# Optimization experiments

Measured on AMD Instinct MI355X. Metric: run time of the kernel, lower is better.

## Reference

```python
import jax, jax.numpy as jnp
import numpy as np

NEG_BIG = -9e15  # matches torch -9000000000000000.0

def setup_inputs() -> dict:
    key = jax.random.key(0)
    k1, k2, k3, k4 = jax.random.split(key, 4)
    B, N, F_IN, F_OUT = 8, 2048, 128, 64
    x = jax.random.normal(k1, (B, N, F_IN), dtype=jnp.float32)
    adj = jax.random.randint(k2, (B, N, N), 0, 2, dtype=jnp.int32)
    # xavier_uniform-style init for params
    limW = float(np.sqrt(6.0 / (F_IN + F_OUT)))
    W = jax.random.uniform(k3, (F_IN, F_OUT), minval=-limW, maxval=limW, dtype=jnp.float32)
    lima = float(np.sqrt(6.0 / (2 * F_OUT + 1)))
    a = jax.random.uniform(k4, (2 * F_OUT, 1), minval=-lima, maxval=lima, dtype=jnp.float32)
    return {"x": x, "adj": adj, "W": W, "a": a}

def reference(x, adj, W, a):
    # x: [B, N, F_in], adj: [B, N, N], W: [F_in, F_out], a: [2*F_out, 1]
    h = jnp.einsum('bnf,fo->bno', x, W)            # [B, N, F_out]
    F_out = W.shape[1]
    # The repeat/cat construction computes a_input[b,i,j] = [h_i ; h_j], so
    # a_input @ a decomposes into f1_i + f2_j without the O(N^2 * 2F) tensor.
    f1 = h @ a[:F_out, 0]                          # [B, N]
    f2 = h @ a[F_out:, 0]                          # [B, N]
    e = jnp.tanh(f1[:, :, None] + f2[:, None, :])  # [B, N, N]
    att = jnp.where(adj > 0, e, NEG_BIG)
    att = jax.nn.softmax(att, axis=2)              # [B, N, N]
    h_prime = jnp.einsum('bmn,bno->bmo', att, h)   # [B, N, F_out]
    return jax.nn.elu(h_prime)                     # concat=True branch
```

## Files before the change

kernel.cpp:

```cpp
#include <hip/hip_runtime.h>
#include <math.h>

#define BB 8
#define NN 2048
#define FIN 128
#define FOUT 64
#define TI 16
#define TJ 512
#define TJP (TJ + 8)
#define NTILE (NN / TJ)

typedef short bf16x8 __attribute__((ext_vector_type(8)));
typedef float f32x4 __attribute__((ext_vector_type(4)));

__device__ __forceinline__ float exp_tanh(float z) {
    float zc = fminf(fmaxf(z, -15.f), 15.f);
    float u = __expf(zc + zc);
    float tn = (u - 1.f) * __builtin_amdgcn_rcpf(u + 1.f);
    return __expf(tn);
}

__device__ __forceinline__ unsigned short f2bf(float x) {
    union { float f; unsigned u; } v; v.f = x;
    unsigned r = v.u + 0x7FFF + ((v.u >> 16) & 1);
    return (unsigned short)(r >> 16);
}

__global__ __launch_bounds__(256, 2) void gat_k1(const float* __restrict__ x,
                                                 const float* __restrict__ W,
                                                 const float* __restrict__ a,
                                                 unsigned short* __restrict__ ht,
                                                 float* __restrict__ f1,
                                                 float* __restrict__ f2) {
    __shared__ __attribute__((aligned(16))) float Wl[FIN][FOUT];
    __shared__ __attribute__((aligned(16))) float xs[16][FIN];
    int t = threadIdx.x;

    const float4* W4 = (const float4*)W;
    float4* Wl4 = (float4*)&Wl[0][0];
#pragma unroll
    for (int kk = 0; kk < 8; ++kk) Wl4[t + 256 * kk] = W4[t + 256 * kk];

    size_t row0 = (size_t)blockIdx.x * 16;
    const float4* x4 = (const float4*)(x + row0 * FIN);
    float4* xs4 = (float4*)&xs[0][0];
#pragma unroll
    for (int kk = 0; kk < 2; ++kk) xs4[t + 256 * kk] = x4[t + 256 * kk];
    __syncthreads();

    int c = t & 63;
    int rq = t >> 6;
    float acc[4] = {0.f, 0.f, 0.f, 0.f};
#pragma unroll 8
    for (int k = 0; k < FIN; ++k) {
        float wv = Wl[k][c];
        acc[0] = fmaf(xs[rq][k], wv, acc[0]);
        acc[1] = fmaf(xs[rq + 4][k], wv, acc[1]);
        acc[2] = fmaf(xs[rq + 8][k], wv, acc[2]);
        acc[3] = fmaf(xs[rq + 12][k], wv, acc[3]);
    }
    float a1c = a[c], a2c = a[FOUT + c];
#pragma unroll
    for (int m = 0; m < 4; ++m) {
        size_t bn = row0 + rq + 4 * m;
        int b = (int)(bn >> 11);
        int n = (int)(bn & 2047);
        ht[((size_t)b * FOUT + c) * NN + n] = f2bf(acc[m]);
        float p1 = acc[m] * a1c;
        float p2 = acc[m] * a2c;
#pragma unroll
        for (int off = 32; off > 0; off >>= 1) {
            p1 += __shfl_down(p1, off, 64);
            p2 += __shfl_down(p2, off, 64);
        }
        if (c == 0) { f1[bn] = p1; f2[bn] = p2; }
    }
}

__global__ __launch_bounds__(256, 4) void gat_k2(const int* __restrict__ adj,
                                                 const unsigned short* __restrict__ ht,
                                                 const float* __restrict__ f1,
                                                 const float* __restrict__ f2,
                                                 float* __restrict__ out) {
    __shared__ __attribute__((aligned(16))) unsigned short pb[TI][TJP];
    __shared__ __attribute__((aligned(16))) float f2s[NN];
    __shared__ float f1s[TI];
    __shared__ float srow[TI][2];

    int t = threadIdx.x;
    int b = blockIdx.y;
    int i0 = blockIdx.x * TI;

    const float* f2b = f2 + (size_t)b * NN;
#pragma unroll
    for (int kk = 0; kk < 2; ++kk)
        ((float4*)f2s)[t + 256 * kk] = ((const float4*)f2b)[t + 256 * kk];
    if (t < TI) f1s[t] = f1[(size_t)b * NN + i0 + t];
    __syncthreads();

    int lane = t & 63;
    int w = t >> 6;
    int mrow = lane & 15;
    int quad = lane >> 4;

    int j4 = t & 127;
    int r0 = t >> 7;

    const int* adjbase = adj + ((size_t)b * NN + (size_t)i0) * NN;
    const int* arow[8];
    float f1r[8];
#pragma unroll
    for (int kk = 0; kk < 8; ++kk) {
        arow[kk] = adjbase + (size_t)(r0 + 2 * kk) * NN + 4 * j4;
        f1r[kk] = f1s[r0 + 2 * kk];
    }

    const unsigned short* hrow =
        ht + ((size_t)b * FOUT + w * 16 + mrow) * NN + 8 * quad;
    const unsigned short* prow = &pb[mrow][8 * quad];

    f32x4 acc = {0.f, 0.f, 0.f, 0.f};
    float ps[8] = {0.f, 0.f, 0.f, 0.f, 0.f, 0.f, 0.f, 0.f};

    for (int tile = 0; tile < NTILE; ++tile) {
        int j0 = tile * TJ;
        float4 fv = ((const float4*)(f2s + j0))[j4];
#pragma unroll
        for (int kk = 0; kk < 8; ++kk) {
            int4 av = *(const int4*)(arow[kk] + j0);
            float f1i = f1r[kk];
            float4 p;
            p.x = (av.x > 0) ? exp_tanh(f1i + fv.x) : 0.f;
            p.y = (av.y > 0) ? exp_tanh(f1i + fv.y) : 0.f;
            p.z = (av.z > 0) ? exp_tanh(f1i + fv.z) : 0.f;
            p.w = (av.w > 0) ? exp_tanh(f1i + fv.w) : 0.f;
            ps[kk] += p.x + p.y + p.z + p.w;
            ushort4 pk;
            pk.x = f2bf(p.x); pk.y = f2bf(p.y);
            pk.z = f2bf(p.z); pk.w = f2bf(p.w);
            *(ushort4*)&pb[r0 + 2 * kk][4 * j4] = pk;
        }
        __syncthreads();
        const unsigned short* hp = hrow + j0;
#pragma unroll 4
        for (int ch = 0; ch < TJ / 32; ++ch) {
            bf16x8 af = *(const bf16x8*)(prow + 32 * ch);
            bf16x8 bf = *(const bf16x8*)(hp + 32 * ch);
            acc = __builtin_amdgcn_mfma_f32_16x16x32_bf16(af, bf, acc, 0, 0, 0);
        }
        __syncthreads();
    }

#pragma unroll
    for (int kk = 0; kk < 8; ++kk) {
        float s = ps[kk];
#pragma unroll
        for (int off = 32; off > 0; off >>= 1) s += __shfl_down(s, off, 64);
        if (lane == 0) srow[2 * kk + (w >> 1)][w & 1] = s;
    }
    __syncthreads();
    float* ob = out + ((size_t)b * NN + (size_t)i0) * FOUT + w * 16 + mrow;
#pragma unroll
    for (int u = 0; u < 4; ++u) {
        int row = quad * 4 + u;
        float rs = srow[row][0] + srow[row][1];
        float s = acc[u] / rs;
        ob[(size_t)row * FOUT] = (s > 0.f) ? s : expm1f(s);
    }
}

extern "C" void kernel_launch(void* const* d_in, const int* in_sizes, int n_in,
                              void* d_out, int out_size, void* d_ws, size_t ws_size,
                              hipStream_t stream) {
    const float* x   = (const float*)d_in[0];
    const int*   adj = (const int*)d_in[1];
    const float* W   = (const float*)d_in[2];
    const float* a   = (const float*)d_in[3];
    float* out = (float*)d_out;

    unsigned short* ht = (unsigned short*)d_ws;
    float* f1 = (float*)(ht + (size_t)BB * FOUT * NN);
    float* f2 = f1 + (size_t)BB * NN;

    gat_k1<<<dim3(BB * NN / 16), dim3(256), 0, stream>>>(x, W, a, ht, f1, f2);
    gat_k2<<<dim3(NN / TI, BB), dim3(256), 0, stream>>>(adj, ht, f1, f2, out);
}
```

Baseline: 239.4 us.

## Split attention over column tiles across blocks with atomic accumulation and epilogue kernel

After: 233.2 us. 2.6% less time.

```diff
diff --git a/kernel.cpp b/kernel.cpp
--- a/kernel.cpp
+++ b/kernel.cpp
@@ -81,22 +81,16 @@
                                                  const unsigned short* __restrict__ ht,
                                                  const float* __restrict__ f1,
                                                  const float* __restrict__ f2,
-                                                 float* __restrict__ out) {
+                                                 float* __restrict__ accg,
+                                                 float* __restrict__ rs) {
     __shared__ __attribute__((aligned(16))) unsigned short pb[TI][TJP];
-    __shared__ __attribute__((aligned(16))) float f2s[NN];
+    __shared__ __attribute__((aligned(16))) float f2s[TJ];
     __shared__ float f1s[TI];
-    __shared__ float srow[TI][2];
 
     int t = threadIdx.x;
-    int b = blockIdx.y;
     int i0 = blockIdx.x * TI;
-
-    const float* f2b = f2 + (size_t)b * NN;
-#pragma unroll
-    for (int kk = 0; kk < 2; ++kk)
-        ((float4*)f2s)[t + 256 * kk] = ((const float4*)f2b)[t + 256 * kk];
-    if (t < TI) f1s[t] = f1[(size_t)b * NN + i0 + t];
-    __syncthreads();
+    int j0 = blockIdx.y * TJ;
+    int b = blockIdx.z;
 
     int lane = t & 63;
     int w = t >> 6;
@@ -106,49 +100,48 @@
     int j4 = t & 127;
     int r0 = t >> 7;
 
-    const int* adjbase = adj + ((size_t)b * NN + (size_t)i0) * NN;
-    const int* arow[8];
+    const int* adjbase = adj + (((size_t)b * NN + i0) * NN) + j0 + 4 * j4;
+    int4 avreg[8];
+#pragma unroll
+    for (int kk = 0; kk < 8; ++kk)
+        avreg[kk] = *(const int4*)(adjbase + (size_t)(r0 + 2 * kk) * NN);
+
+    ((float2*)f2s)[t] = ((const float2*)(f2 + (size_t)b * NN + j0))[t];
+    if (t < TI) f1s[t] = f1[(size_t)b * NN + i0 + t];
+    __syncthreads();
+
     float f1r[8];
 #pragma unroll
+    for (int kk = 0; kk < 8; ++kk) f1r[kk] = f1s[r0 + 2 * kk];
+
+    float4 fv = ((const float4*)f2s)[j4];
+    float ps[8];
+#pragma unroll
     for (int kk = 0; kk < 8; ++kk) {
-        arow[kk] = adjbase + (size_t)(r0 + 2 * kk) * NN + 4 * j4;
-        f1r[kk] = f1s[r0 + 2 * kk];
+        int4 av = avreg[kk];
+        float f1i = f1r[kk];
+        float4 p;
+        p.x = (av.x > 0) ? exp_tanh(f1i + fv.x) : 0.f;
+        p.y = (av.y > 0) ? exp_tanh(f1i + fv.y) : 0.f;
+        p.z = (av.z > 0) ? exp_tanh(f1i + fv.z) : 0.f;
+        p.w = (av.w > 0) ? exp_tanh(f1i + fv.w) : 0.f;
+        ps[kk] = p.x + p.y + p.z + p.w;
+        ushort4 pk;
+        pk.x = f2bf(p.x); pk.y = f2bf(p.y);
+        pk.z = f2bf(p.z); pk.w = f2bf(p.w);
+        *(ushort4*)&pb[r0 + 2 * kk][4 * j4] = pk;
     }
+    __syncthreads();
 
-    const unsigned short* hrow =
-        ht + ((size_t)b * FOUT + w * 16 + mrow) * NN + 8 * quad;
+    const unsigned short* hp =
+        ht + ((size_t)b * FOUT + w * 16 + mrow) * NN + j0 + 8 * quad;
     const unsigned short* prow = &pb[mrow][8 * quad];
-
     f32x4 acc = {0.f, 0.f, 0.f, 0.f};
-    float ps[8] = {0.f, 0.f, 0.f, 0.f, 0.f, 0.f, 0.f, 0.f};
-
-    for (int tile = 0; tile < NTILE; ++tile) {
-        int j0 = tile * TJ;
-        float4 fv = ((const float4*)(f2s + j0))[j4];
-#pragma unroll
-        for (int kk = 0; kk < 8; ++kk) {
-            int4 av = *(const int4*)(arow[kk] + j0);
-            float f1i = f1r[kk];
-            float4 p;
-            p.x = (av.x > 0) ? exp_tanh(f1i + fv.x) : 0.f;
-            p.y = (av.y > 0) ? exp_tanh(f1i + fv.y) : 0.f;
-            p.z = (av.z > 0) ? exp_tanh(f1i + fv.z) : 0.f;
-            p.w = (av.w > 0) ? exp_tanh(f1i + fv.w) : 0.f;
-            ps[kk] += p.x + p.y + p.z + p.w;
-            ushort4 pk;
-            pk.x = f2bf(p.x); pk.y = f2bf(p.y);
-            pk.z = f2bf(p.z); pk.w = f2bf(p.w);
-            *(ushort4*)&pb[r0 + 2 * kk][4 * j4] = pk;
-        }
-        __syncthreads();
-        const unsigned short* hp = hrow + j0;
 #pragma unroll 4
-        for (int ch = 0; ch < TJ / 32; ++ch) {
-            bf16x8 af = *(const bf16x8*)(prow + 32 * ch);
-            bf16x8 bf = *(const bf16x8*)(hp + 32 * ch);
-            acc = __builtin_amdgcn_mfma_f32_16x16x32_bf16(af, bf, acc, 0, 0, 0);
-        }
-        __syncthreads();
+    for (int ch = 0; ch < TJ / 32; ++ch) {
+        bf16x8 af = *(const bf16x8*)(prow + 32 * ch);
+        bf16x8 bf = *(const bf16x8*)(hp + 32 * ch);
+        acc = __builtin_amdgcn_mfma_f32_16x16x32_bf16(af, bf, acc, 0, 0, 0);
     }
 
 #pragma unroll
@@ -156,17 +149,30 @@
         float s = ps[kk];
 #pragma unroll
         for (int off = 32; off > 0; off >>= 1) s += __shfl_down(s, off, 64);
-        if (lane == 0) srow[2 * kk + (w >> 1)][w & 1] = s;
+        if (lane == 0)
+            atomicAdd(&rs[(size_t)b * NN + i0 + r0 + 2 * kk], s);
     }
-    __syncthreads();
-    float* ob = out + ((size_t)b * NN + (size_t)i0) * FOUT + w * 16 + mrow;
+    float* ap = accg + ((size_t)b * NN + i0) * FOUT + w * 16 + mrow;
 #pragma unroll
     for (int u = 0; u < 4; ++u) {
         int row = quad * 4 + u;
-        float rs = srow[row][0] + srow[row][1];
-        float s = acc[u] / rs;
-        ob[(size_t)row * FOUT] = (s > 0.f) ? s : expm1f(s);
+        atomicAdd(&ap[(size_t)row * FOUT], acc[u]);
     }
+}
+
+__global__ __launch_bounds__(256) void gat_k3(const float* __restrict__ accg,
+                                              const float* __restrict__ rs,
+                                              float* __restrict__ out) {
+    int g4 = blockIdx.x * 256 + threadIdx.x;
+    int row = g4 >> 4;
+    float rinv = __builtin_amdgcn_rcpf(rs[row]);
+    float4 v = ((const float4*)accg)[g4];
+    float4 o;
+    float sx = v.x * rinv; o.x = (sx > 0.f) ? sx : expm1f(sx);
+    float sy = v.y * rinv; o.y = (sy > 0.f) ? sy : expm1f(sy);
+    float sz = v.z * rinv; o.z = (sz > 0.f) ? sz : expm1f(sz);
+    float sw = v.w * rinv; o.w = (sw > 0.f) ? sw : expm1f(sw);
+    ((float4*)out)[g4] = o;
 }
 
 extern "C" void kernel_launch(void* const* d_in, const int* in_sizes, int n_in,
@@ -179,9 +185,13 @@
     float* out = (float*)d_out;
 
     unsigned short* ht = (unsigned short*)d_ws;
-    float* f1 = (float*)(ht + (size_t)BB * FOUT * NN);
-    float* f2 = f1 + (size_t)BB * NN;
+    float* f1   = (float*)(ht + (size_t)BB * FOUT * NN);
+    float* f2   = f1 + (size_t)BB * NN;
+    float* accg = f2 + (size_t)BB * NN;
+    float* rs   = accg + (size_t)BB * NN * FOUT;
+    hipMemsetAsync(accg, 0, ((size_t)BB * NN * FOUT + (size_t)BB * NN) * 4, stream);
 
     gat_k1<<<dim3(BB * NN / 16), dim3(256), 0, stream>>>(x, W, a, ht, f1, f2);
-    gat_k2<<<dim3(NN / TI, BB), dim3(256), 0, stream>>>(adj, ht, f1, f2, out);
+    gat_k2<<<dim3(NN / TI, NTILE, BB), dim3(256), 0, stream>>>(adj, ht, f1, f2, accg, rs);
+    gat_k3<<<dim3(BB * NN * FOUT / 1024), dim3(256), 0, stream>>>(accg, rs, out);
 }
```
